# Performance work log

Hardware: AMD Instinct MI355X
Metric: run time of the kernel (lower is better)

The kernel has to match this reference:

```python
import jax, jax.numpy as jnp
import numpy as np

N_NODES = 100000
N_EDGES = 3200000
N_GRAPHS = 512
IN_DIM = 29   # NUM_COMPONENT_TYPES(15) + NUM_PARAMS(14)
HID = 128
LAT = 256


def setup_inputs() -> dict:
    key = jax.random.key(0)
    ks = jax.random.split(key, 16)
    x = jax.random.normal(ks[0], (N_NODES, IN_DIM), dtype=jnp.float32)
    edge_index = jax.random.randint(ks[1], (2, N_EDGES), 0, N_NODES, dtype=jnp.int64)
    batch = jnp.sort(jax.random.randint(ks[2], (N_NODES,), 0, N_GRAPHS, dtype=jnp.int64))

    def lin(k, fan_in, fan_out):
        kw, kb = jax.random.split(k)
        s = 1.0 / np.sqrt(fan_in)
        W = jax.random.uniform(kw, (fan_in, fan_out), minval=-s, maxval=s, dtype=jnp.float32)
        b = jax.random.uniform(kb, (fan_out,), minval=-s, maxval=s, dtype=jnp.float32)
        return W, b

    W1, b1 = lin(ks[3], IN_DIM, HID)
    W2, b2 = lin(ks[4], HID, HID)
    W3, b3 = lin(ks[5], HID, HID)
    Wmu, bmu = lin(ks[6], HID, LAT)
    Wlv, blv = lin(ks[7], HID, LAT)
    return {"x": x, "edge_index": edge_index, "batch": batch,
            "W1": W1, "b1": b1, "W2": W2, "b2": b2, "W3": W3, "b3": b3,
            "Wmu": Wmu, "bmu": bmu, "Wlv": Wlv, "blv": blv}


def _gcn_conv(h, W, b, src, dst, dis):
    # PyG GCNConv: out = D^-1/2 (A + I) D^-1/2 (h W) + b
    hw = h @ W                                   # [N, out]
    norm = dis[src] * dis[dst]                   # [E]
    agg = jax.ops.segment_sum(hw[src] * norm[:, None], dst, num_segments=h.shape[0])
    return agg + hw * (dis * dis)[:, None] + b   # self-loop term has norm dis[i]^2


def reference(x, edge_index, batch, W1, b1, W2, b2, W3, b3, Wmu, bmu, Wlv, blv):
    src, dst = edge_index[0], edge_index[1]
    # symmetric degree with self-loops (computed once, identical across layers)
    deg = jax.ops.segment_sum(jnp.ones(src.shape[0], jnp.float32), dst,
                              num_segments=x.shape[0]) + 1.0
    dis = jax.lax.rsqrt(deg)

    h = jax.nn.relu(_gcn_conv(x, W1, b1, src, dst, dis))
    h = jax.nn.relu(_gcn_conv(h, W2, b2, src, dst, dis))
    h = jax.nn.relu(_gcn_conv(h, W3, b3, src, dst, dis))

    # global_mean_pool over graph ids
    sums = jax.ops.segment_sum(h, batch, num_segments=N_GRAPHS)
    cnts = jax.ops.segment_sum(jnp.ones(h.shape[0], jnp.float32), batch,
                               num_segments=N_GRAPHS)
    pooled = sums / jnp.maximum(cnts, 1.0)[:, None]   # [G, HID]

    mu = pooled @ Wmu + bmu
    logvar = pooled @ Wlv + blv
    return (mu, logvar)
```

## Files before the change

### kernel.cpp

```cpp
#include <hip/hip_runtime.h>
#include <hip/hip_bf16.h>

#define N_NODES 100000
#define N_EDGES 3200000
#define N_GRAPHS 512
#define IN_DIM 29
#define HID 128
#define LAT 256
#define NB 391
#define CAP 9216

typedef unsigned int uint;
typedef unsigned short ushort;
typedef float v4f __attribute__((ext_vector_type(4)));
typedef short v8s __attribute__((ext_vector_type(8)));

__device__ __forceinline__ ushort f2bf(float f) {
    uint u = __float_as_uint(f);
    return (ushort)((u + 0x7FFFu + ((u >> 16) & 1u)) >> 16);
}
__device__ __forceinline__ float bf2f(ushort h) { return __uint_as_float(((uint)h) << 16); }
__device__ __forceinline__ float bf_lo(uint p) { return __uint_as_float(p << 16); }
__device__ __forceinline__ float bf_hi(uint p) { return __uint_as_float(p & 0xFFFF0000u); }
__device__ __forceinline__ uint pack2(float a, float b) {
    return (uint)f2bf(a) | ((uint)f2bf(b) << 16);
}

__device__ __forceinline__ void bfadd(float* a, uint4 q) {
    a[0] += bf_lo(q.x); a[1] += bf_hi(q.x);
    a[2] += bf_lo(q.y); a[3] += bf_hi(q.y);
    a[4] += bf_lo(q.z); a[5] += bf_hi(q.z);
    a[6] += bf_lo(q.w); a[7] += bf_hi(q.w);
}


__global__ __launch_bounds__(1024, 2) void k_binA(const int* __restrict__ src, const int* __restrict__ dst,
                                                  int* __restrict__ bktCnt, int* __restrict__ packed, int e) {
    __shared__ int hist[NB];
    __shared__ int base[NB];
    int t = threadIdx.x;
    for (int i = t; i < NB; i += 1024) hist[i] = 0;
    __syncthreads();
    int d[8], s[8];
    const int blockStart = blockIdx.x * 8192;
    #pragma unroll
    for (int k = 0; k < 8; ++k) {
        int idx = blockStart + k * 1024 + t;
        if (idx < e) {
            d[k] = dst[idx];
            s[k] = src[idx];
            atomicAdd(&hist[d[k] >> 8], 1);
        } else d[k] = -1;
    }
    __syncthreads();
    for (int i = t; i < NB; i += 1024) {
        int c = hist[i];
        base[i] = c ? atomicAdd(&bktCnt[i], c) : 0;
    }
    __syncthreads();
    #pragma unroll
    for (int k = 0; k < 8; ++k) {
        if (d[k] >= 0) {
            int b = d[k] >> 8;
            int pos = atomicAdd(&base[b], 1);
            if (pos < CAP) packed[b * CAP + pos] = ((d[k] & 255) << 17) | s[k];
        }
    }
}

__global__ __launch_bounds__(512) void k_bscan(const int* __restrict__ bktCnt, int* __restrict__ colStart) {
    __shared__ int sh[512];
    int t = threadIdx.x;
    int v = (t < NB) ? bktCnt[t] : 0;
    if (v > CAP) v = CAP;
    sh[t] = v;
    __syncthreads();
    for (int off = 1; off < 512; off <<= 1) {
        int x = (t >= off) ? sh[t - off] : 0;
        __syncthreads();
        sh[t] += x;
        __syncthreads();
    }
    int excl = sh[t] - v;
    if (t <= NB) colStart[t] = excl;
}

__global__ __launch_bounds__(1024, 2) void k_binB(const int* __restrict__ bktCnt, const int* __restrict__ colStart,
                                                  const int* __restrict__ packed, int* __restrict__ col,
                                                  int* __restrict__ rp, float* __restrict__ dis, int n) {
    __shared__ int cnt[8192];
    __shared__ int sh[1024];
    const int b = blockIdx.x;
    int cntB = bktCnt[b];
    if (cntB > CAP) cntB = CAP;
    const int segS = b * CAP;
    const int colBase = colStart[b];
    int t = threadIdx.x;
    #pragma unroll
    for (int k = 0; k < 8; ++k) cnt[t + k * 1024] = 0;
    __syncthreads();
    for (int j = t; j < cntB; j += 1024) {
        int pk = packed[segS + j];
        int key = ((pk >> 17) << 5) | ((pk & 0x1FFFF) >> 12);
        atomicAdd(&cnt[key], 1);
    }
    __syncthreads();
    int base8 = t << 3;
    int v[8];
    int sum = 0;
    #pragma unroll
    for (int k = 0; k < 8; ++k) { v[k] = cnt[base8 + k]; sum += v[k]; }
    sh[t] = sum;
    __syncthreads();
    for (int off = 1; off < 1024; off <<= 1) {
        int x = (t >= off) ? sh[t - off] : 0;
        __syncthreads();
        sh[t] += x;
        __syncthreads();
    }
    int run = colBase + sh[t] - sum;
    #pragma unroll
    for (int k = 0; k < 8; ++k) { cnt[base8 + k] = run; run += v[k]; }
    __syncthreads();
    if (t < 256) {
        int node = (b << 8) + t;
        int start = cnt[t << 5];
        int next = (t == 255) ? (colBase + cntB) : cnt[(t + 1) << 5];
        int deg = next - start;
        if (node <= n) rp[node] = start;
        if (node < n) dis[node] = rsqrtf((float)deg + 1.0f);
    }
    __syncthreads();
    for (int j = t; j < cntB; j += 1024) {
        int pk = packed[segS + j];
        int key = ((pk >> 17) << 5) | ((pk & 0x1FFFF) >> 12);
        int pos = atomicAdd(&cnt[key], 1);
        col[pos] = pk & 0x1FFFF;
    }
}


__device__ __forceinline__ void pack_one(const float* W, ushort* hi, ushort* lo, int Ksrc, int idx) {
    int j = idx & 7;
    int lane = (idx >> 3) & 63;
    int nt = (idx >> 9) & 7;
    int ks = idx >> 12;
    int k = ks * 32 + (lane >> 4) * 8 + j;
    int n = nt * 16 + (lane & 15);
    float v = (k < Ksrc) ? W[k * 128 + n] : 0.f;
    ushort h = f2bf(v);
    ushort l = f2bf(v - bf2f(h));
    hi[idx] = h;
    lo[idx] = l;
}

__global__ __launch_bounds__(256) void k_pack_all(const float* __restrict__ W1, const float* __restrict__ W2,
                                                  const float* __restrict__ W3,
                                                  ushort* w1h, ushort* w1l, ushort* w2h, ushort* w2l,
                                                  ushort* w3h, ushort* w3l, int* __restrict__ bktCnt) {
    int idx = blockIdx.x * 256 + threadIdx.x;
    if (idx < NB) bktCnt[idx] = 0;
    if (idx < 4096) {
        pack_one(W1, w1h, w1l, IN_DIM, idx);
    } else if (idx < 4096 + 16384) {
        pack_one(W2, w2h, w2l, HID, idx - 4096);
    } else if (idx < 4096 + 32768) {
        pack_one(W3, w3h, w3l, HID, idx - 4096 - 16384);
    }
}


__global__ __launch_bounds__(256, 6) void k_gemm_mfma_f32(const float* __restrict__ in,
                                                          const ushort* __restrict__ Whi,
                                                          const ushort* __restrict__ Wlo,
                                                          const float* __restrict__ dis,
                                                          ushort* __restrict__ out, int n) {
    const int wave = threadIdx.x >> 6;
    const int lane = threadIdx.x & 63;
    const int m0 = (blockIdx.x * 4 + wave) * 16;
    if (m0 >= n) return;
    int row = m0 + (lane & 15);
    if (row >= n) row = n - 1;
    const int kh = (lane >> 4) * 8;
    const float* rptr = in + (size_t)row * IN_DIM + kh;

    v4f acc[8];
    #pragma unroll
    for (int t = 0; t < 8; ++t) acc[t] = (v4f){0.f, 0.f, 0.f, 0.f};

    float a[8];
    #pragma unroll
    for (int j = 0; j < 8; ++j) a[j] = (kh + j < IN_DIM) ? rptr[j] : 0.f;
    v8s ahi, alo;
    #pragma unroll
    for (int j = 0; j < 8; ++j) {
        ushort h = f2bf(a[j]);
        ushort l = f2bf(a[j] - bf2f(h));
        ahi[j] = (short)h;
        alo[j] = (short)l;
    }
    const ushort* bh = Whi + (size_t)lane * 8;
    const ushort* bl = Wlo + (size_t)lane * 8;
    #pragma unroll
    for (int nt = 0; nt < 8; ++nt) {
        v8s bhi = *(const v8s*)(bh + nt * 512);
        v8s blo = *(const v8s*)(bl + nt * 512);
        acc[nt] = __builtin_amdgcn_mfma_f32_16x16x32_bf16(ahi, bhi, acc[nt], 0, 0, 0);
        acc[nt] = __builtin_amdgcn_mfma_f32_16x16x32_bf16(ahi, blo, acc[nt], 0, 0, 0);
        acc[nt] = __builtin_amdgcn_mfma_f32_16x16x32_bf16(alo, bhi, acc[nt], 0, 0, 0);
    }

    const int orow0 = m0 + (lane >> 4) * 4;
    const int col0 = lane & 15;
    #pragma unroll
    for (int r = 0; r < 4; ++r) {
        int orow = orow0 + r;
        if (orow < n) {
            float dv = dis[orow];
            #pragma unroll
            for (int nt = 0; nt < 8; ++nt)
                out[(size_t)orow * 128 + nt * 16 + col0] = f2bf(acc[nt][r] * dv);
        }
    }
}


__global__ __launch_bounds__(256, 6) void k_gemm_mfma_bf(const ushort* __restrict__ in,
                                                         const ushort* __restrict__ Whi,
                                                         const ushort* __restrict__ Wlo,
                                                         const float* __restrict__ dis,
                                                         ushort* __restrict__ out, int n) {
    const int wave = threadIdx.x >> 6;
    const int lane = threadIdx.x & 63;
    const int m0 = (blockIdx.x * 4 + wave) * 16;
    if (m0 >= n) return;
    int row = m0 + (lane & 15);
    if (row >= n) row = n - 1;
    const int kh = (lane >> 4) * 8;
    const ushort* rptr = in + (size_t)row * 128 + kh;

    v4f acc[8];
    #pragma unroll
    for (int t = 0; t < 8; ++t) acc[t] = (v4f){0.f, 0.f, 0.f, 0.f};

    #pragma unroll
    for (int ks = 0; ks < 4; ++ks) {
        v8s a = *(const v8s*)(rptr + ks * 32);
        const ushort* bh = Whi + (size_t)(ks * 8) * 512 + (size_t)lane * 8;
        const ushort* bl = Wlo + (size_t)(ks * 8) * 512 + (size_t)lane * 8;
        #pragma unroll
        for (int nt = 0; nt < 8; ++nt) {
            v8s bhi = *(const v8s*)(bh + nt * 512);
            v8s blo = *(const v8s*)(bl + nt * 512);
            acc[nt] = __builtin_amdgcn_mfma_f32_16x16x32_bf16(a, bhi, acc[nt], 0, 0, 0);
            acc[nt] = __builtin_amdgcn_mfma_f32_16x16x32_bf16(a, blo, acc[nt], 0, 0, 0);
        }
    }

    const int orow0 = m0 + (lane >> 4) * 4;
    const int col0 = lane & 15;
    #pragma unroll
    for (int r = 0; r < 4; ++r) {
        int orow = orow0 + r;
        if (orow < n) {
            float dv = dis[orow];
            #pragma unroll
            for (int nt = 0; nt < 8; ++nt)
                out[(size_t)orow * 128 + nt * 16 + col0] = f2bf(acc[nt][r] * dv);
        }
    }
}


__global__ __launch_bounds__(256, 6) void k_agg(const ushort* __restrict__ hws, const int* __restrict__ rp,
                                                const int* __restrict__ col, const float* __restrict__ dis,
                                                const float* __restrict__ bias, ushort* __restrict__ out, int n) {
    int g = blockIdx.x * 32 + (threadIdx.x >> 3);
    int node = (g < n) ? g : g - n;
    if (g >= 2 * n) return;
    int c8 = ((g < n) ? 0 : 64) + ((threadIdx.x & 7) << 3);
    int s = rp[node], e = rp[node + 1];
    float A[8] = {0.f, 0.f, 0.f, 0.f, 0.f, 0.f, 0.f, 0.f};
    float B[8] = {0.f, 0.f, 0.f, 0.f, 0.f, 0.f, 0.f, 0.f};
    int j = s;
    for (; j + 7 < e; j += 8) {
        int c0 = col[j],     c1 = col[j + 1], c2 = col[j + 2], c3 = col[j + 3];
        int c4 = col[j + 4], c5 = col[j + 5], c6 = col[j + 6], c7 = col[j + 7];
        uint4 q0 = *(const uint4*)(hws + ((size_t)c0 << 7) + c8);
        uint4 q1 = *(const uint4*)(hws + ((size_t)c1 << 7) + c8);
        uint4 q2 = *(const uint4*)(hws + ((size_t)c2 << 7) + c8);
        uint4 q3 = *(const uint4*)(hws + ((size_t)c3 << 7) + c8);
        uint4 q4 = *(const uint4*)(hws + ((size_t)c4 << 7) + c8);
        uint4 q5 = *(const uint4*)(hws + ((size_t)c5 << 7) + c8);
        uint4 q6 = *(const uint4*)(hws + ((size_t)c6 << 7) + c8);
        uint4 q7 = *(const uint4*)(hws + ((size_t)c7 << 7) + c8);
        bfadd(A, q0); bfadd(B, q1); bfadd(A, q2); bfadd(B, q3);
        bfadd(A, q4); bfadd(B, q5); bfadd(A, q6); bfadd(B, q7);
    }
    if (j + 3 < e) {
        int c0 = col[j], c1 = col[j + 1], c2 = col[j + 2], c3 = col[j + 3];
        uint4 q0 = *(const uint4*)(hws + ((size_t)c0 << 7) + c8);
        uint4 q1 = *(const uint4*)(hws + ((size_t)c1 << 7) + c8);
        uint4 q2 = *(const uint4*)(hws + ((size_t)c2 << 7) + c8);
        uint4 q3 = *(const uint4*)(hws + ((size_t)c3 << 7) + c8);
        bfadd(A, q0); bfadd(B, q1); bfadd(A, q2); bfadd(B, q3);
        j += 4;
    }
    for (; j < e; ++j) {
        int c = col[j];
        uint4 q = *(const uint4*)(hws + ((size_t)c << 7) + c8);
        bfadd(A, q);
    }
    uint4 qs = *(const uint4*)(hws + ((size_t)node << 7) + c8);
    bfadd(A, qs);
    float dv = dis[node];
    float4 bv0 = *(const float4*)(bias + c8);
    float4 bv1 = *(const float4*)(bias + c8 + 4);
    float r0 = fmaxf(dv * (A[0] + B[0]) + bv0.x, 0.f);
    float r1 = fmaxf(dv * (A[1] + B[1]) + bv0.y, 0.f);
    float r2 = fmaxf(dv * (A[2] + B[2]) + bv0.z, 0.f);
    float r3 = fmaxf(dv * (A[3] + B[3]) + bv0.w, 0.f);
    float r4 = fmaxf(dv * (A[4] + B[4]) + bv1.x, 0.f);
    float r5 = fmaxf(dv * (A[5] + B[5]) + bv1.y, 0.f);
    float r6 = fmaxf(dv * (A[6] + B[6]) + bv1.z, 0.f);
    float r7 = fmaxf(dv * (A[7] + B[7]) + bv1.w, 0.f);
    uint4 o;
    o.x = pack2(r0, r1);
    o.y = pack2(r2, r3);
    o.z = pack2(r4, r5);
    o.w = pack2(r6, r7);
    *(uint4*)(out + (size_t)node * 128 + c8) = o;
}


__global__ __launch_bounds__(256) void k_pool_head(const ushort* __restrict__ h, const int* __restrict__ batch,
                                                   const float* __restrict__ Wmu, const float* __restrict__ bmu,
                                                   const float* __restrict__ Wlv, const float* __restrict__ blv,
                                                   float* __restrict__ out, int n) {
    int g = blockIdx.x;
    int t = threadIdx.x;
    int lo = 0, hi = n;
    while (lo < hi) { int m = (lo + hi) >> 1; if (batch[m] < g) lo = m + 1; else hi = m; }
    int start = lo;
    hi = n;
    while (lo < hi) { int m = (lo + hi) >> 1; if (batch[m] < g + 1) lo = m + 1; else hi = m; }
    int end = lo;

    __shared__ float sh0[256];
    __shared__ float sh1[256];
    __shared__ float pooled[128];
    int lane = t & 63;
    int grp = t >> 6;
    float a0 = 0.f, a1 = 0.f;
    for (int i = start + grp; i < end; i += 4) {
        uint q = *(const uint*)(h + (size_t)i * 128 + lane * 2);
        a0 += bf_lo(q);
        a1 += bf_hi(q);
    }
    sh0[t] = a0;
    sh1[t] = a1;
    __syncthreads();
    if (t < 64) {
        float cnt = (float)(end - start);
        float inv = 1.0f / fmaxf(cnt, 1.0f);
        float s0 = sh0[t] + sh0[t + 64] + sh0[t + 128] + sh0[t + 192];
        float s1 = sh1[t] + sh1[t + 64] + sh1[t + 128] + sh1[t + 192];
        pooled[t * 2] = s0 * inv;
        pooled[t * 2 + 1] = s1 * inv;
    }
    __syncthreads();
    float amu = bmu[t], alv = blv[t];
    for (int k = 0; k < 128; k += 4) {
        float p0 = pooled[k], p1 = pooled[k + 1], p2 = pooled[k + 2], p3 = pooled[k + 3];
        amu += p0 * Wmu[(k + 0) * 256 + t] + p1 * Wmu[(k + 1) * 256 + t]
             + p2 * Wmu[(k + 2) * 256 + t] + p3 * Wmu[(k + 3) * 256 + t];
        alv += p0 * Wlv[(k + 0) * 256 + t] + p1 * Wlv[(k + 1) * 256 + t]
             + p2 * Wlv[(k + 2) * 256 + t] + p3 * Wlv[(k + 3) * 256 + t];
    }
    out[(size_t)g * 256 + t] = amu;
    out[(size_t)N_GRAPHS * 256 + (size_t)g * 256 + t] = alv;
}


extern "C" void kernel_launch(void* const* d_in, const int* in_sizes, int n_in,
                              void* d_out, int out_size, void* d_ws, size_t ws_size,
                              hipStream_t stream) {
    const float* x    = (const float*)d_in[0];
    const int*   eidx = (const int*)d_in[1];
    const int*   batch= (const int*)d_in[2];
    const float* W1   = (const float*)d_in[3];
    const float* b1   = (const float*)d_in[4];
    const float* W2   = (const float*)d_in[5];
    const float* b2   = (const float*)d_in[6];
    const float* W3   = (const float*)d_in[7];
    const float* b3   = (const float*)d_in[8];
    const float* Wmu  = (const float*)d_in[9];
    const float* bmu  = (const float*)d_in[10];
    const float* Wlv  = (const float*)d_in[11];
    const float* blv  = (const float*)d_in[12];
    float* out = (float*)d_out;

    const int N = N_NODES, E = N_EDGES;
    const int* srcp = eidx;
    const int* dstp = eidx + E;

    ushort* w1h = (ushort*)d_ws;
    ushort* w1l = w1h + 4096;
    ushort* w2h = w1l + 4096;
    ushort* w2l = w2h + 16384;
    ushort* w3h = w2l + 16384;
    ushort* w3l = w3h + 16384;
    ushort* A   = w3l + 16384;
    ushort* B   = A + (size_t)N * 128;
    float*  dis = (float*)(B + (size_t)N * 128);
    int*   rp   = (int*)(dis + N);
    int*   bktCnt   = rp + (N + 2);
    int*   colStart = bktCnt + 512;
    int*   packed = colStart + 512;
    int*   col    = packed + (size_t)NB * CAP;

    const int gE8192 = (E + 8191) / 8192;

    k_pack_all<<<144, 256, 0, stream>>>(W1, W2, W3, w1h, w1l, w2h, w2l, w3h, w3l, bktCnt);

    k_binA<<<gE8192, 1024, 0, stream>>>(srcp, dstp, bktCnt, packed, E);
    k_bscan<<<1, 512, 0, stream>>>(bktCnt, colStart);
    k_binB<<<NB, 1024, 0, stream>>>(bktCnt, colStart, packed, col, rp, dis, N);

    const int gGemm = (N + 63) / 64;
    const int gAgg  = (2 * N + 31) / 32;

    k_gemm_mfma_f32<<<gGemm, 256, 0, stream>>>(x, w1h, w1l, dis, A, N);
    k_agg<<<gAgg, 256, 0, stream>>>(A, rp, col, dis, b1, B, N);
    k_gemm_mfma_bf<<<gGemm, 256, 0, stream>>>(B, w2h, w2l, dis, A, N);
    k_agg<<<gAgg, 256, 0, stream>>>(A, rp, col, dis, b2, B, N);
    k_gemm_mfma_bf<<<gGemm, 256, 0, stream>>>(B, w3h, w3l, dis, A, N);
    k_agg<<<gAgg, 256, 0, stream>>>(A, rp, col, dis, b3, B, N);
    k_pool_head<<<N_GRAPHS, 256, 0, stream>>>(B, batch, Wmu, bmu, Wlv, blv, out, N);
}
```

Baseline: 520.1 us.

## Aggregate layer-1 on 29-dim input before GEMM instead of 128-dim output

New measurement: 482.8 us. 1.08x faster.

```diff
diff --git a/kernel.cpp b/kernel.cpp
--- a/kernel.cpp
+++ b/kernel.cpp
@@ -170,11 +170,63 @@
 }
 
 
-__global__ __launch_bounds__(256, 6) void k_gemm_mfma_f32(const float* __restrict__ in,
-                                                          const ushort* __restrict__ Whi,
-                                                          const ushort* __restrict__ Wlo,
-                                                          const float* __restrict__ dis,
-                                                          ushort* __restrict__ out, int n) {
+__global__ __launch_bounds__(256) void k_scale(const float* __restrict__ x, const float* __restrict__ dis,
+                                               float* __restrict__ xt, int n) {
+    int idx = blockIdx.x * 256 + threadIdx.x;
+    if (idx >= n * 32) return;
+    int row = idx >> 5, k = idx & 31;
+    float v = (k < IN_DIM) ? x[(size_t)row * IN_DIM + k] * dis[row] : 0.f;
+    xt[idx] = v;
+}
+
+__global__ __launch_bounds__(256, 6) void k_agg29(const float* __restrict__ xt, const int* __restrict__ rp,
+                                                  const int* __restrict__ col, const float* __restrict__ dis,
+                                                  float* __restrict__ y, int n) {
+    int node = (int)((blockIdx.x * 256 + threadIdx.x) >> 3);
+    if (node >= n) return;
+    int c4 = (threadIdx.x & 7) << 2;
+    int s = rp[node], e = rp[node + 1];
+    v4f A = (v4f){0.f, 0.f, 0.f, 0.f};
+    v4f B = (v4f){0.f, 0.f, 0.f, 0.f};
+    int j = s;
+    for (; j + 7 < e; j += 8) {
+        int c0 = col[j],     c1 = col[j + 1], c2 = col[j + 2], c3 = col[j + 3];
+        int c4i = col[j + 4], c5 = col[j + 5], c6 = col[j + 6], c7 = col[j + 7];
+        v4f q0 = *(const v4f*)(xt + ((size_t)c0 << 5) + c4);
+        v4f q1 = *(const v4f*)(xt + ((size_t)c1 << 5) + c4);
+        v4f q2 = *(const v4f*)(xt + ((size_t)c2 << 5) + c4);
+        v4f q3 = *(const v4f*)(xt + ((size_t)c3 << 5) + c4);
+        v4f q4 = *(const v4f*)(xt + ((size_t)c4i << 5) + c4);
+        v4f q5 = *(const v4f*)(xt + ((size_t)c5 << 5) + c4);
+        v4f q6 = *(const v4f*)(xt + ((size_t)c6 << 5) + c4);
+        v4f q7 = *(const v4f*)(xt + ((size_t)c7 << 5) + c4);
+        A += q0; B += q1; A += q2; B += q3;
+        A += q4; B += q5; A += q6; B += q7;
+    }
+    if (j + 3 < e) {
+        int c0 = col[j], c1 = col[j + 1], c2 = col[j + 2], c3 = col[j + 3];
+        v4f q0 = *(const v4f*)(xt + ((size_t)c0 << 5) + c4);
+        v4f q1 = *(const v4f*)(xt + ((size_t)c1 << 5) + c4);
+        v4f q2 = *(const v4f*)(xt + ((size_t)c2 << 5) + c4);
+        v4f q3 = *(const v4f*)(xt + ((size_t)c3 << 5) + c4);
+        A += q0; B += q1; A += q2; B += q3;
+        j += 4;
+    }
+    for (; j < e; ++j) {
+        int c = col[j];
+        A += *(const v4f*)(xt + ((size_t)c << 5) + c4);
+    }
+    A += *(const v4f*)(xt + ((size_t)node << 5) + c4);
+    float dv = dis[node];
+    v4f o = (A + B) * dv;
+    *(v4f*)(y + ((size_t)node << 5) + c4) = o;
+}
+
+__global__ __launch_bounds__(256, 6) void k_gemm1(const float* __restrict__ in,
+                                                  const ushort* __restrict__ Whi,
+                                                  const ushort* __restrict__ Wlo,
+                                                  const float* __restrict__ bias,
+                                                  ushort* __restrict__ out, int n) {
     const int wave = threadIdx.x >> 6;
     const int lane = threadIdx.x & 63;
     const int m0 = (blockIdx.x * 4 + wave) * 16;
@@ -182,7 +234,7 @@
     int row = m0 + (lane & 15);
     if (row >= n) row = n - 1;
     const int kh = (lane >> 4) * 8;
-    const float* rptr = in + (size_t)row * IN_DIM + kh;
+    const float* rptr = in + ((size_t)row << 5) + kh;
 
     v4f acc[8];
     #pragma unroll
@@ -190,7 +242,7 @@
 
     float a[8];
     #pragma unroll
-    for (int j = 0; j < 8; ++j) a[j] = (kh + j < IN_DIM) ? rptr[j] : 0.f;
+    for (int j = 0; j < 8; ++j) a[j] = rptr[j];
     v8s ahi, alo;
     #pragma unroll
     for (int j = 0; j < 8; ++j) {
@@ -212,14 +264,16 @@
 
     const int orow0 = m0 + (lane >> 4) * 4;
     const int col0 = lane & 15;
+    float bb[8];
+    #pragma unroll
+    for (int nt = 0; nt < 8; ++nt) bb[nt] = bias[nt * 16 + col0];
     #pragma unroll
     for (int r = 0; r < 4; ++r) {
         int orow = orow0 + r;
         if (orow < n) {
-            float dv = dis[orow];
             #pragma unroll
             for (int nt = 0; nt < 8; ++nt)
-                out[(size_t)orow * 128 + nt * 16 + col0] = f2bf(acc[nt][r] * dv);
+                out[(size_t)orow * 128 + nt * 16 + col0] = f2bf(fmaxf(acc[nt][r] + bb[nt], 0.f));
         }
     }
 }
@@ -419,6 +473,9 @@
     int*   packed = colStart + 512;
     int*   col    = packed + (size_t)NB * CAP;
 
+    float* xt = (float*)A;
+    float* yv = xt + (size_t)N * 32;
+
     const int gE8192 = (E + 8191) / 8192;
 
     k_pack_all<<<144, 256, 0, stream>>>(W1, W2, W3, w1h, w1l, w2h, w2l, w3h, w3l, bktCnt);
@@ -430,8 +487,10 @@
     const int gGemm = (N + 63) / 64;
     const int gAgg  = (2 * N + 31) / 32;
 
-    k_gemm_mfma_f32<<<gGemm, 256, 0, stream>>>(x, w1h, w1l, dis, A, N);
-    k_agg<<<gAgg, 256, 0, stream>>>(A, rp, col, dis, b1, B, N);
+    k_scale<<<(N * 32 + 255) / 256, 256, 0, stream>>>(x, dis, xt, N);
+    k_agg29<<<(N * 8 + 255) / 256, 256, 0, stream>>>(xt, rp, col, dis, yv, N);
+    k_gemm1<<<gGemm, 256, 0, stream>>>(yv, w1h, w1l, b1, B, N);
+
     k_gemm_mfma_bf<<<gGemm, 256, 0, stream>>>(B, w2h, w2l, dis, A, N);
     k_agg<<<gAgg, 256, 0, stream>>>(A, rp, col, dis, b2, B, N);
     k_gemm_mfma_bf<<<gGemm, 256, 0, stream>>>(B, w3h, w3l, dis, A, N);
```
